# Kernel tuning notes

Hardware: AMD Instinct MI355X
Metric: run time of the kernel (lower is better)

Reference implementation:

```python
import jax, jax.numpy as jnp
import numpy as np

EMBED_DIM = 1024
N_HEADS = 16
HEAD_DIM = EMBED_DIM // N_HEADS


def setup_inputs() -> dict:
    key = jax.random.key(0)
    ks = jax.random.split(key, 9)
    s = 1.0 / np.sqrt(EMBED_DIM)
    x = jax.random.normal(ks[0], (4, 2048, EMBED_DIM), dtype=jnp.float32)
    Wq = jax.random.uniform(ks[1], (EMBED_DIM, EMBED_DIM), jnp.float32, -s, s)
    bq = jax.random.uniform(ks[2], (EMBED_DIM,), jnp.float32, -s, s)
    Wk = jax.random.uniform(ks[3], (EMBED_DIM, EMBED_DIM), jnp.float32, -s, s)
    bk = jax.random.uniform(ks[4], (EMBED_DIM,), jnp.float32, -s, s)
    Wv = jax.random.uniform(ks[5], (EMBED_DIM, EMBED_DIM), jnp.float32, -s, s)
    bv = jax.random.uniform(ks[6], (EMBED_DIM,), jnp.float32, -s, s)
    Wo = jax.random.uniform(ks[7], (EMBED_DIM, EMBED_DIM), jnp.float32, -s, s)
    bo = jax.random.uniform(ks[8], (EMBED_DIM,), jnp.float32, -s, s)
    return {"x": x, "Wq": Wq, "bq": bq, "Wk": Wk, "bk": bk,
            "Wv": Wv, "bv": bv, "Wo": Wo, "bo": bo}


def reference(x, Wq, bq, Wk, bk, Wv, bv, Wo, bo):
    B, S, _ = x.shape
    # projections (PyTorch Linear: x @ W.T + b; weights stored as [in,out] here)
    q = x @ Wq + bq
    k = x @ Wk + bk
    v = x @ Wv + bv
    # [B, H, S, D]
    q = q.reshape(B, S, N_HEADS, HEAD_DIM).transpose(0, 2, 1, 3)
    k = k.reshape(B, S, N_HEADS, HEAD_DIM).transpose(0, 2, 1, 3)
    v = v.reshape(B, S, N_HEADS, HEAD_DIM).transpose(0, 2, 1, 3)
    scores = jnp.einsum('bhsd,bhtd->bhst', q, k) / np.sqrt(HEAD_DIM).astype(np.float32)
    attn = jax.nn.softmax(scores, axis=-1)
    out = jnp.einsum('bhst,bhtd->bhsd', attn, v)
    out = out.transpose(0, 2, 1, 3).reshape(B, S, EMBED_DIM)
    return out @ Wo + bo  # dropout=0 (eval) -> identity
```

## Files before the change

### kernel.cpp

```cpp
#include <hip/hip_runtime.h>
#include <stdint.h>

#define EMBED 1024
#define NH 16
#define HD 64
#define SEQ 2048
#define BATCH 4
#define M_TOT (BATCH*SEQ)
#define QSCALE 0.18033688011112042f

typedef __attribute__((ext_vector_type(8))) short short8;
typedef __attribute__((ext_vector_type(4))) float floatx4;
typedef __attribute__((ext_vector_type(4))) unsigned int uintx4;

__device__ __forceinline__ unsigned short f2bf(float f) {
    union { float f; unsigned int u; } v; v.f = f;
    unsigned int r = v.u + 0x7fffu + ((v.u >> 16) & 1u);
    return (unsigned short)(r >> 16);
}

__device__ __forceinline__ void load_lds16(const unsigned short* g, unsigned short* l) {
    __builtin_amdgcn_global_load_lds(
        (const __attribute__((address_space(1))) unsigned int*)g,
        (__attribute__((address_space(3))) unsigned int*)l, 16, 0, 0);
}

__global__ void cvt_x(const float* __restrict__ x, unsigned short* __restrict__ xb) {
    int i = (blockIdx.x * 256 + threadIdx.x) * 4;
    float4 v = *(const float4*)(x + i);
    ushort4 o;
    o.x = f2bf(v.x); o.y = f2bf(v.y); o.z = f2bf(v.z); o.w = f2bf(v.w);
    *(ushort4*)(xb + i) = o;
}

__global__ void wtrans(const float* __restrict__ w0, const float* __restrict__ w1,
                       const float* __restrict__ w2, const float* __restrict__ w3,
                       unsigned short* __restrict__ t0, unsigned short* __restrict__ t1,
                       unsigned short* __restrict__ t2, unsigned short* __restrict__ t3) {
    __shared__ float tile[32][33];
    const float* W; unsigned short* T;
    switch (blockIdx.z) { case 0: W=w0; T=t0; break; case 1: W=w1; T=t1; break;
                          case 2: W=w2; T=t2; break; default: W=w3; T=t3; }
    int n0 = blockIdx.x * 32, k0 = blockIdx.y * 32;
    int tx = threadIdx.x, ty = threadIdx.y;
    #pragma unroll
    for (int i = 0; i < 4; i++)
        tile[ty + i*8][tx] = W[(k0 + ty + i*8) * EMBED + n0 + tx];
    __syncthreads();
    #pragma unroll
    for (int i = 0; i < 4; i++)
        T[(n0 + ty + i*8) * EMBED + k0 + tx] = f2bf(tile[tx][ty + i*8]);
}

#define ST_AH(buf_, kt_, h_) do { \
    const unsigned short* s_ = Asrc + (kt_)*64 + (h_)*64*EMBED; \
    unsigned short* d_ = ldst + (buf_)*32768 + (h_)*4096; \
    load_lds16(s_,              d_); \
    load_lds16(s_ + 128*EMBED,  d_ + 8192); \
  } while(0)
#define ST_BH(buf_, kt_, h_) do { \
    const unsigned short* s_ = Bsrc + (kt_)*64 + (h_)*32*EMBED; \
    unsigned short* d_ = bdst + (buf_)*32768 + (h_)*2048; \
    load_lds16(s_,              d_); \
    load_lds16(s_ + 128*EMBED,  d_ + 8192); \
  } while(0)

template<int MO, int NO>
__device__ __forceinline__ void mfma_quad(floatx4 (&acc)[8][4],
        const short8 (&a)[4][2], const short8 (&b)[2][2]) {
    #pragma unroll
    for (int k=0;k<2;k++)
      #pragma unroll
      for (int m=0;m<4;m++)
        #pragma unroll
        for (int n=0;n<2;n++)
          acc[MO+m][NO+n] = __builtin_amdgcn_mfma_f32_16x16x32_bf16(a[m][k], b[n][k], acc[MO+m][NO+n], 0,0,0);
}

template<bool B1, bool T2, int WAITN>
__device__ __forceinline__ void ktile(int t, int buf,
        const unsigned short* Abase, const unsigned short* Bbase,
        const unsigned short* Asrc, const unsigned short* Bsrc,
        unsigned short* ldst, unsigned short* bdst,
        int cs0, int cs1, floatx4 (&acc)[8][4]) {
    const unsigned short* Ab = Abase + buf*32768;
    const unsigned short* Bb = Bbase + buf*32768;
    short8 fA[4][2], fBlo[2][2], fBhi[2][2];
    #pragma unroll
    for (int i=0;i<4;i++) {
        fA[i][0] = *(const short8*)(Ab + i*1024 + cs0);
        fA[i][1] = *(const short8*)(Ab + i*1024 + cs1);
    }
    #pragma unroll
    for (int n=0;n<2;n++) {
        fBlo[n][0] = *(const short8*)(Bb + n*1024 + cs0);
        fBlo[n][1] = *(const short8*)(Bb + n*1024 + cs1);
    }
    if (B1) ST_BH(buf^1, t+1, 1);
    asm volatile("s_waitcnt lgkmcnt(8)");
    __builtin_amdgcn_s_barrier();
    asm volatile("s_waitcnt lgkmcnt(0)");
    __builtin_amdgcn_s_setprio(1);
    mfma_quad<0,0>(acc, fA, fBlo);
    __builtin_amdgcn_s_setprio(0);
    __builtin_amdgcn_s_barrier();
    #pragma unroll
    for (int n=0;n<2;n++) {
        fBhi[n][0] = *(const short8*)(Bb + (2+n)*1024 + cs0);
        fBhi[n][1] = *(const short8*)(Bb + (2+n)*1024 + cs1);
    }
    if (T2) ST_AH(buf, t+2, 0);
    __builtin_amdgcn_s_barrier();
    asm volatile("s_waitcnt lgkmcnt(0)");
    __builtin_amdgcn_s_setprio(1);
    mfma_quad<0,2>(acc, fA, fBhi);
    __builtin_amdgcn_s_setprio(0);
    __builtin_amdgcn_s_barrier();
    #pragma unroll
    for (int i=0;i<4;i++) {
        fA[i][0] = *(const short8*)(Ab + (4+i)*1024 + cs0);
        fA[i][1] = *(const short8*)(Ab + (4+i)*1024 + cs1);
    }
    if (T2) ST_BH(buf, t+2, 0);
    __builtin_amdgcn_s_barrier();
    asm volatile("s_waitcnt lgkmcnt(0)");
    __builtin_amdgcn_s_setprio(1);
    mfma_quad<4,2>(acc, fA, fBhi);
    __builtin_amdgcn_s_setprio(0);
    __builtin_amdgcn_s_barrier();
    if (T2) ST_AH(buf, t+2, 1);
    __builtin_amdgcn_s_setprio(1);
    mfma_quad<4,0>(acc, fA, fBlo);
    __builtin_amdgcn_s_setprio(0);
    if (WAITN == 6)      { asm volatile("s_waitcnt vmcnt(6)" ::: "memory"); }
    else if (WAITN == 0) { asm volatile("s_waitcnt vmcnt(0)" ::: "memory"); }
    __builtin_amdgcn_s_barrier();
}

__global__ __launch_bounds__(512, 2) void gemm8(
        const unsigned short* __restrict__ A, const unsigned short* __restrict__ BT,
        const float* __restrict__ b0, const float* __restrict__ b1, const float* __restrict__ b2,
        void* __restrict__ o0, void* __restrict__ o1, void* __restrict__ o2, int mode) {
    __shared__ unsigned short lds[2*32768];
    const int tid = threadIdx.x;
    const int lane = tid & 63, wave = tid >> 6;
    const int quad = lane >> 4, l16 = lane & 15;
    const int wm = wave >> 2, wn = wave & 3;
    const int id = blockIdx.x;
    const int xcd = id & 7, j = id >> 3;
    const int mblk = (xcd * 4 + (j & 3)) * 256;
    const int nblk = (j >> 2) * 256;

    const int srow = tid >> 3;
    const int scol = ((tid & 7) ^ (srow & 7)) * 8;
    const int brow = (srow & 31) + ((srow >> 5) << 6);
    const unsigned short* Asrc = A  + (size_t)(mblk + srow) * EMBED + scol;
    const unsigned short* Bsrc = BT + (size_t)(nblk + brow) * EMBED + scol;
    unsigned short* ldst = lds + wave * 512;
    unsigned short* bdst = lds + 16384 + (wave & 3)*512 + (wave >> 2)*4096;

    const int cs0 = ( quad      ^ (l16 & 7)) * 8;
    const int cs1 = ((quad ^ 4) ^ (l16 & 7)) * 8;
    const unsigned short* Abase = lds + (wm*128 + l16)*64;
    const unsigned short* Bbase = lds + 16384 + (wn*64 + l16)*64;

    floatx4 acc[8][4];
    #pragma unroll
    for (int m=0;m<8;m++)
      #pragma unroll
      for (int n=0;n<4;n++) acc[m][n] = (floatx4){0.f,0.f,0.f,0.f};

    ST_AH(0,0,0); ST_BH(0,0,0); ST_BH(0,0,1); ST_AH(0,0,1);
    asm volatile("s_waitcnt vmcnt(4)" ::: "memory");
    ST_AH(1,1,0); ST_BH(1,1,0); ST_AH(1,1,1);
    asm volatile("s_waitcnt vmcnt(6)" ::: "memory");
    __builtin_amdgcn_s_barrier();

    #pragma unroll 2
    for (int t = 0; t < 14; ++t)
        ktile<true, true, 6>(t, t & 1, Abase, Bbase, Asrc, Bsrc, ldst, bdst, cs0, cs1, acc);
    ktile<true,  false, 0>(14, 0, Abase, Bbase, Asrc, Bsrc, ldst, bdst, cs0, cs1, acc);
    ktile<false, false, -1>(15, 1, Abase, Bbase, Asrc, Bsrc, ldst, bdst, cs0, cs1, acc);

    if (mode == 1) {
        float* O = (float*)o0;
        #pragma unroll
        for (int mt=0;mt<8;mt++)
          #pragma unroll
          for (int nt=0;nt<4;nt++) {
            int col = nblk + wn*64 + nt*16 + l16;
            float bv = b0[col];
            #pragma unroll
            for (int r=0;r<4;r++) {
                int row = mblk + wm*128 + mt*16 + quad*4 + r;
                O[(size_t)row * EMBED + col] = acc[mt][nt][r] + bv;
            }
          }
    } else {
        int which = nblk >> 10;
        const float* bs = (which==0) ? b0 : (which==1) ? b1 : b2;
        unsigned short* O = (unsigned short*)((which==0) ? o0 : (which==1) ? o1 : o2);
        #pragma unroll
        for (int mt=0;mt<8;mt++)
          #pragma unroll
          for (int nt=0;nt<4;nt++) {
            int coll = (nblk & 1023) + wn*64 + nt*16 + l16;
            float bv = bs[coll];
            int h = coll >> 6, d = coll & 63;
            #pragma unroll
            for (int r=0;r<4;r++) {
                int row = mblk + wm*128 + mt*16 + quad*4 + r;
                int b = row >> 11, s = row & 2047;
                float v = acc[mt][nt][r] + bv;
                if (which == 0) {
                    v *= QSCALE;
                    O[((size_t)(b*NH + h)*SEQ + s)*HD + d] = f2bf(v);
                } else if (which == 1) {
                    O[((size_t)(b*NH + h)*SEQ + s)*HD + d] = f2bf(v);
                } else {
                    int sp = (s & ~31) | (((s >> 2) & 3) << 3) | (((s >> 4) & 1) << 2) | (s & 3);
                    O[((size_t)(b*NH + h)*HD + d)*SEQ + sp] = f2bf(v);
                }
            }
          }
    }
}

__global__ __launch_bounds__(512, 4) void attn(
    const unsigned short* __restrict__ Q, const unsigned short* __restrict__ K,
    const unsigned short* __restrict__ VTp, unsigned short* __restrict__ O) {
    __shared__ unsigned short kv[2][4096];
    unsigned short* kvf = &kv[0][0];
    int tid = threadIdx.x;
    int lane = tid & 63, wave = tid >> 6;
    int quad = lane >> 4, l16 = lane & 15;
    int id = blockIdx.x;
    int bh = (id & 7) * 8 + (id >> 6);
    int qblk = (id >> 3) & 7;
    int b = bh >> 4, h = bh & 15;
    int q0 = qblk * 256 + wave * 32;
    const unsigned short* Qb = Q + (size_t)bh * SEQ * HD;
    const unsigned short* Kb = K + (size_t)bh * SEQ * HD;
    const unsigned short* Vb = VTp + (size_t)bh * HD * SEQ;
    int li = (wave & 3) * 64 + lane;
    const unsigned short* src;
    int dstofs = (wave & 3) * 512 + ((wave >> 2) ? 2048 : 0);
    int src_step;
    if (wave < 4) {
        int t = li >> 3, slot = li & 7;
        int dblk = slot ^ (t & 7);
        src = Kb + (size_t)t * HD + dblk * 8;
        src_step = 32 * HD;
    } else {
        int d = li >> 2, slot = li & 3;
        int swz = (d & 3) ^ ((d >> 2) & 3);
        src = Vb + (size_t)d * SEQ + (slot ^ swz) * 8;
        src_step = 32;
    }
    short8 qf[2][2];
    #pragma unroll
    for (int mt=0;mt<2;mt++) {
        const unsigned short* qp = Qb + (size_t)(q0 + mt*16 + l16) * HD + quad*8;
        qf[mt][0] = *(const short8*)(qp);
        qf[mt][1] = *(const short8*)(qp + 32);
    }
    floatx4 o_acc[2][4], l_acc[2];
    #pragma unroll
    for (int mt=0;mt<2;mt++) {
        l_acc[mt] = (floatx4){0.f,0.f,0.f,0.f};
        #pragma unroll
        for (int dt=0;dt<4;dt++) o_acc[mt][dt] = (floatx4){0.f,0.f,0.f,0.f};
    }
    short8 ones;
    #pragma unroll
    for (int jj=0;jj<8;jj++) ones[jj] = (short)0x3F80;
    int koff[2][2], voff[4];
    #pragma unroll
    for (int nt=0;nt<2;nt++) {
        int t = nt*16 + l16;
        #pragma unroll
        for (int hh=0;hh<2;hh++)
            koff[nt][hh] = t*64 + ((hh*4 + quad) ^ (t & 7)) * 8;
    }
    #pragma unroll
    for (int dt=0;dt<4;dt++) {
        int d = dt*16 + l16;
        voff[dt] = 2048 + d*32 + ((quad ^ (d & 3) ^ ((d >> 2) & 3))) * 8;
    }

    load_lds16(src, kvf + dstofs);
    src += src_step;

    for (int it = 0; it < 64; ++it) {
        const unsigned short* kb = kvf + (it & 1) * 4096;
        if (it < 63) {
            load_lds16(src, kvf + ((it & 1) ^ 1) * 4096 + dstofs);
            src += src_step;
            asm volatile("s_waitcnt vmcnt(1)" ::: "memory");
        } else {
            asm volatile("s_waitcnt vmcnt(0)" ::: "memory");
        }
        __builtin_amdgcn_s_barrier();
        asm volatile("" ::: "memory");
        short8 kf[2][2], vf[4];
        #pragma unroll
        for (int nt=0;nt<2;nt++) {
            kf[nt][0] = *(const short8*)(kb + koff[nt][0]);
            kf[nt][1] = *(const short8*)(kb + koff[nt][1]);
        }
        #pragma unroll
        for (int dt=0;dt<4;dt++)
            vf[dt] = *(const short8*)(kb + voff[dt]);
        floatx4 sacc[2][2];
        __builtin_amdgcn_s_setprio(1);
        #pragma unroll
        for (int nt=0;nt<2;nt++)
          #pragma unroll
          for (int mt=0;mt<2;mt++) {
            floatx4 s = (floatx4){0.f,0.f,0.f,0.f};
            s = __builtin_amdgcn_mfma_f32_16x16x32_bf16(kf[nt][0], qf[mt][0], s, 0, 0, 0);
            s = __builtin_amdgcn_mfma_f32_16x16x32_bf16(kf[nt][1], qf[mt][1], s, 0, 0, 0);
            sacc[nt][mt] = s;
          }
        __builtin_amdgcn_s_setprio(0);
        short8 pf[2];
        #pragma unroll
        for (int mt=0;mt<2;mt++) {
            uintx4 pu;
            #pragma unroll
            for (int jp=0;jp<4;jp++) {
                int nt = jp >> 1, rp = (jp & 1) * 2;
                union { float f; unsigned int u; } e0, e1;
                e0.f = __builtin_amdgcn_exp2f(sacc[nt][mt][rp]);
                e1.f = __builtin_amdgcn_exp2f(sacc[nt][mt][rp+1]);
                pu[jp] = ((e1.u + 0x8000u) & 0xFFFF0000u) | ((e0.u + 0x8000u) >> 16);
            }
            pf[mt] = __builtin_bit_cast(short8, pu);
        }
        __builtin_amdgcn_s_setprio(1);
        #pragma unroll
        for (int mt=0;mt<2;mt++) {
            l_acc[mt] = __builtin_amdgcn_mfma_f32_16x16x32_bf16(ones, pf[mt], l_acc[mt], 0, 0, 0);
            #pragma unroll
            for (int dt=0;dt<4;dt++)
                o_acc[mt][dt] = __builtin_amdgcn_mfma_f32_16x16x32_bf16(vf[dt], pf[mt], o_acc[mt][dt], 0, 0, 0);
        }
        __builtin_amdgcn_s_setprio(0);
        asm volatile("" ::: "memory");
        __builtin_amdgcn_s_barrier();
    }
    #pragma unroll
    for (int mt=0;mt<2;mt++) {
        float inv = 1.f / l_acc[mt][0];
        int s = q0 + mt*16 + l16;
        #pragma unroll
        for (int dt=0;dt<4;dt++) {
            ushort4 w;
            w.x = f2bf(o_acc[mt][dt][0]*inv);
            w.y = f2bf(o_acc[mt][dt][1]*inv);
            w.z = f2bf(o_acc[mt][dt][2]*inv);
            w.w = f2bf(o_acc[mt][dt][3]*inv);
            *(ushort4*)(O + ((size_t)b*SEQ + s)*EMBED + h*HD + dt*16 + quad*4) = w;
        }
    }
}

extern "C" void kernel_launch(void* const* d_in, const int* in_sizes, int n_in,
                              void* d_out, int out_size, void* d_ws, size_t ws_size,
                              hipStream_t stream) {
    const float* x  = (const float*)d_in[0];
    const float* Wq = (const float*)d_in[1]; const float* bq = (const float*)d_in[2];
    const float* Wk = (const float*)d_in[3]; const float* bk = (const float*)d_in[4];
    const float* Wv = (const float*)d_in[5]; const float* bv = (const float*)d_in[6];
    const float* Wo = (const float*)d_in[7]; const float* bo = (const float*)d_in[8];
    char* ws = (char*)d_ws;
    unsigned short* xb  = (unsigned short*)(ws);
    unsigned short* WqT = (unsigned short*)(ws + (16ull<<20));
    unsigned short* WkT = (unsigned short*)(ws + (18ull<<20));
    unsigned short* WvT = (unsigned short*)(ws + (20ull<<20));
    unsigned short* WoT = (unsigned short*)(ws + (22ull<<20));
    unsigned short* Qb  = (unsigned short*)(ws + (24ull<<20));
    unsigned short* Kb  = (unsigned short*)(ws + (40ull<<20));
    unsigned short* VTb = (unsigned short*)(ws + (56ull<<20));
    unsigned short* Ob  = xb;

    cvt_x<<<(M_TOT*EMBED)/1024, 256, 0, stream>>>(x, xb);
    wtrans<<<dim3(32,32,4), dim3(32,8), 0, stream>>>(Wq,Wk,Wv,Wo, WqT,WkT,WvT,WoT);
    gemm8<<<dim3(384), 512, 0, stream>>>(xb, WqT, bq, bk, bv, Qb, Kb, VTb, 0);
    attn<<<dim3(512), 512, 0, stream>>>(Qb, Kb, VTb, Ob);
    gemm8<<<dim3(128), 512, 0, stream>>>(Ob, WoT, bo, bo, bo, (float*)d_out, nullptr, nullptr, 1);
}
```

Measured before the change: 289.1 us.

## Rewrite projection GEMM with 32-wide K tiles, 4-stage LDS ring, LDS-staged V transpose

The GEMM main loop now uses K-steps of 32 over a 4-buffer LDS ring with 3 tiles in flight. Each step takes a single vmcnt wait and barrier, replacing the old 64-wide double-buffered loop with its many interleaved barriers and setprio phases. The V-projection epilogue now writes its transposed, permuted output through an LDS staging tile so global stores are coalesced 16-byte vectors instead of scattered 2-byte writes. The mode is also made a template parameter. The cost is more loop iterations and a changed swizzle, and the new LDS bank pattern or load issue could hurt MFMA overlap.

```diff
diff --git a/kernel.cpp b/kernel.cpp
--- a/kernel.cpp
+++ b/kernel.cpp
@@ -52,96 +52,47 @@
         T[(n0 + ty + i*8) * EMBED + k0 + tx] = f2bf(tile[tx][ty + i*8]);
 }
 
-#define ST_AH(buf_, kt_, h_) do { \
-    const unsigned short* s_ = Asrc + (kt_)*64 + (h_)*64*EMBED; \
-    unsigned short* d_ = ldst + (buf_)*32768 + (h_)*4096; \
-    load_lds16(s_,              d_); \
-    load_lds16(s_ + 128*EMBED,  d_ + 8192); \
+#define ST32(kt_) do { \
+    const int b_ = (kt_) & 3; \
+    const unsigned short* sa_ = Asrc + (kt_)*32; \
+    const unsigned short* sb_ = Bsrc + (kt_)*32; \
+    unsigned short* da_ = ldstA + b_*16384; \
+    unsigned short* db_ = ldstB + b_*16384; \
+    load_lds16(sa_,             da_); \
+    load_lds16(sa_ + 128*EMBED, da_ + 4096); \
+    load_lds16(sb_,             db_); \
+    load_lds16(sb_ + 128*EMBED, db_ + 4096); \
   } while(0)
-#define ST_BH(buf_, kt_, h_) do { \
-    const unsigned short* s_ = Bsrc + (kt_)*64 + (h_)*32*EMBED; \
-    unsigned short* d_ = bdst + (buf_)*32768 + (h_)*2048; \
-    load_lds16(s_,              d_); \
-    load_lds16(s_ + 128*EMBED,  d_ + 8192); \
-  } while(0)
-
-template<int MO, int NO>
-__device__ __forceinline__ void mfma_quad(floatx4 (&acc)[8][4],
-        const short8 (&a)[4][2], const short8 (&b)[2][2]) {
-    #pragma unroll
-    for (int k=0;k<2;k++)
-      #pragma unroll
-      for (int m=0;m<4;m++)
-        #pragma unroll
-        for (int n=0;n<2;n++)
-          acc[MO+m][NO+n] = __builtin_amdgcn_mfma_f32_16x16x32_bf16(a[m][k], b[n][k], acc[MO+m][NO+n], 0,0,0);
-}
-
-template<bool B1, bool T2, int WAITN>
-__device__ __forceinline__ void ktile(int t, int buf,
+
+template<int WAITN, bool STG>
+__device__ __forceinline__ void kt32(int t,
         const unsigned short* Abase, const unsigned short* Bbase,
         const unsigned short* Asrc, const unsigned short* Bsrc,
-        unsigned short* ldst, unsigned short* bdst,
-        int cs0, int cs1, floatx4 (&acc)[8][4]) {
-    const unsigned short* Ab = Abase + buf*32768;
-    const unsigned short* Bb = Bbase + buf*32768;
-    short8 fA[4][2], fBlo[2][2], fBhi[2][2];
-    #pragma unroll
-    for (int i=0;i<4;i++) {
-        fA[i][0] = *(const short8*)(Ab + i*1024 + cs0);
-        fA[i][1] = *(const short8*)(Ab + i*1024 + cs1);
-    }
-    #pragma unroll
-    for (int n=0;n<2;n++) {
-        fBlo[n][0] = *(const short8*)(Bb + n*1024 + cs0);
-        fBlo[n][1] = *(const short8*)(Bb + n*1024 + cs1);
-    }
-    if (B1) ST_BH(buf^1, t+1, 1);
-    asm volatile("s_waitcnt lgkmcnt(8)");
-    __builtin_amdgcn_s_barrier();
-    asm volatile("s_waitcnt lgkmcnt(0)");
-    __builtin_amdgcn_s_setprio(1);
-    mfma_quad<0,0>(acc, fA, fBlo);
-    __builtin_amdgcn_s_setprio(0);
-    __builtin_amdgcn_s_barrier();
-    #pragma unroll
-    for (int n=0;n<2;n++) {
-        fBhi[n][0] = *(const short8*)(Bb + (2+n)*1024 + cs0);
-        fBhi[n][1] = *(const short8*)(Bb + (2+n)*1024 + cs1);
-    }
-    if (T2) ST_AH(buf, t+2, 0);
-    __builtin_amdgcn_s_barrier();
-    asm volatile("s_waitcnt lgkmcnt(0)");
-    __builtin_amdgcn_s_setprio(1);
-    mfma_quad<0,2>(acc, fA, fBhi);
-    __builtin_amdgcn_s_setprio(0);
-    __builtin_amdgcn_s_barrier();
-    #pragma unroll
-    for (int i=0;i<4;i++) {
-        fA[i][0] = *(const short8*)(Ab + (4+i)*1024 + cs0);
-        fA[i][1] = *(const short8*)(Ab + (4+i)*1024 + cs1);
-    }
-    if (T2) ST_BH(buf, t+2, 0);
-    __builtin_amdgcn_s_barrier();
-    asm volatile("s_waitcnt lgkmcnt(0)");
-    __builtin_amdgcn_s_setprio(1);
-    mfma_quad<4,2>(acc, fA, fBhi);
-    __builtin_amdgcn_s_setprio(0);
-    __builtin_amdgcn_s_barrier();
-    if (T2) ST_AH(buf, t+2, 1);
-    __builtin_amdgcn_s_setprio(1);
-    mfma_quad<4,0>(acc, fA, fBlo);
-    __builtin_amdgcn_s_setprio(0);
-    if (WAITN == 6)      { asm volatile("s_waitcnt vmcnt(6)" ::: "memory"); }
-    else if (WAITN == 0) { asm volatile("s_waitcnt vmcnt(0)" ::: "memory"); }
-    __builtin_amdgcn_s_barrier();
-}
-
-__global__ __launch_bounds__(512, 2) void gemm8(
+        unsigned short* ldstA, unsigned short* ldstB, floatx4 (&acc)[8][4]) {
+    const int bo = (t & 3) * 16384;
+    short8 fA[8], fB[4];
+    #pragma unroll
+    for (int m=0;m<8;m++) fA[m] = *(const short8*)(Abase + bo + m*512);
+    #pragma unroll
+    for (int n=0;n<4;n++) fB[n] = *(const short8*)(Bbase + bo + n*512);
+    if (STG) ST32(t+3);
+    #pragma unroll
+    for (int m=0;m<8;m++)
+      #pragma unroll
+      for (int n=0;n<4;n++)
+        acc[m][n] = __builtin_amdgcn_mfma_f32_16x16x32_bf16(fA[m], fB[n], acc[m][n], 0,0,0);
+    if (WAITN >= 0) {
+        asm volatile("s_waitcnt vmcnt(%0)" :: "i"(WAITN >= 0 ? WAITN : 0) : "memory");
+        asm volatile("s_barrier" ::: "memory");
+    }
+}
+
+template<int MODE>
+__global__ __launch_bounds__(512, 2) void gemm32(
         const unsigned short* __restrict__ A, const unsigned short* __restrict__ BT,
         const float* __restrict__ b0, const float* __restrict__ b1, const float* __restrict__ b2,
-        void* __restrict__ o0, void* __restrict__ o1, void* __restrict__ o2, int mode) {
-    __shared__ unsigned short lds[2*32768];
+        void* __restrict__ o0, void* __restrict__ o1, void* __restrict__ o2) {
+    __shared__ unsigned short lds[4*16384];
     const int tid = threadIdx.x;
     const int lane = tid & 63, wave = tid >> 6;
     const int quad = lane >> 4, l16 = lane & 15;
@@ -151,18 +102,16 @@
     const int mblk = (xcd * 4 + (j & 3)) * 256;
     const int nblk = (j >> 2) * 256;
 
-    const int srow = tid >> 3;
-    const int scol = ((tid & 7) ^ (srow & 7)) * 8;
-    const int brow = (srow & 31) + ((srow >> 5) << 6);
+    const int srow = tid >> 2;
+    const int scol = ((tid & 3) ^ (srow & 3)) * 8;
     const unsigned short* Asrc = A  + (size_t)(mblk + srow) * EMBED + scol;
-    const unsigned short* Bsrc = BT + (size_t)(nblk + brow) * EMBED + scol;
-    unsigned short* ldst = lds + wave * 512;
-    unsigned short* bdst = lds + 16384 + (wave & 3)*512 + (wave >> 2)*4096;
-
-    const int cs0 = ( quad      ^ (l16 & 7)) * 8;
-    const int cs1 = ((quad ^ 4) ^ (l16 & 7)) * 8;
-    const unsigned short* Abase = lds + (wm*128 + l16)*64;
-    const unsigned short* Bbase = lds + 16384 + (wn*64 + l16)*64;
+    const unsigned short* Bsrc = BT + (size_t)(nblk + srow) * EMBED + scol;
+    unsigned short* ldstA = lds + wave * 512;
+    unsigned short* ldstB = lds + 8192 + wave * 512;
+
+    const int cs = (quad ^ (l16 & 3)) * 8;
+    const unsigned short* Abase = lds + (wm*128 + l16)*32 + cs;
+    const unsigned short* Bbase = lds + 8192 + (wn*64 + l16)*32 + cs;
 
     floatx4 acc[8][4];
     #pragma unroll
@@ -170,19 +119,19 @@
       #pragma unroll
       for (int n=0;n<4;n++) acc[m][n] = (floatx4){0.f,0.f,0.f,0.f};
 
-    ST_AH(0,0,0); ST_BH(0,0,0); ST_BH(0,0,1); ST_AH(0,0,1);
-    asm volatile("s_waitcnt vmcnt(4)" ::: "memory");
-    ST_AH(1,1,0); ST_BH(1,1,0); ST_AH(1,1,1);
-    asm volatile("s_waitcnt vmcnt(6)" ::: "memory");
-    __builtin_amdgcn_s_barrier();
-
-    #pragma unroll 2
-    for (int t = 0; t < 14; ++t)
-        ktile<true, true, 6>(t, t & 1, Abase, Bbase, Asrc, Bsrc, ldst, bdst, cs0, cs1, acc);
-    ktile<true,  false, 0>(14, 0, Abase, Bbase, Asrc, Bsrc, ldst, bdst, cs0, cs1, acc);
-    ktile<false, false, -1>(15, 1, Abase, Bbase, Asrc, Bsrc, ldst, bdst, cs0, cs1, acc);
-
-    if (mode == 1) {
+    ST32(0); ST32(1); ST32(2);
+    asm volatile("s_waitcnt vmcnt(8)" ::: "memory");
+    asm volatile("s_barrier" ::: "memory");
+
+    #pragma unroll 4
+    for (int t = 0; t < 28; ++t)
+        kt32<8,true>(t, Abase, Bbase, Asrc, Bsrc, ldstA, ldstB, acc);
+    kt32<8,true >(28, Abase, Bbase, Asrc, Bsrc, ldstA, ldstB, acc);
+    kt32<4,false>(29, Abase, Bbase, Asrc, Bsrc, ldstA, ldstB, acc);
+    kt32<0,false>(30, Abase, Bbase, Asrc, Bsrc, ldstA, ldstB, acc);
+    kt32<-1,false>(31, Abase, Bbase, Asrc, Bsrc, ldstA, ldstB, acc);
+
+    if (MODE == 1) {
         float* O = (float*)o0;
         #pragma unroll
         for (int mt=0;mt<8;mt++)
@@ -199,30 +148,55 @@
     } else {
         int which = nblk >> 10;
         const float* bs = (which==0) ? b0 : (which==1) ? b1 : b2;
-        unsigned short* O = (unsigned short*)((which==0) ? o0 : (which==1) ? o1 : o2);
-        #pragma unroll
-        for (int mt=0;mt<8;mt++)
-          #pragma unroll
-          for (int nt=0;nt<4;nt++) {
-            int coll = (nblk & 1023) + wn*64 + nt*16 + l16;
-            float bv = bs[coll];
-            int h = coll >> 6, d = coll & 63;
-            #pragma unroll
-            for (int r=0;r<4;r++) {
-                int row = mblk + wm*128 + mt*16 + quad*4 + r;
-                int b = row >> 11, s = row & 2047;
-                float v = acc[mt][nt][r] + bv;
-                if (which == 0) {
-                    v *= QSCALE;
-                    O[((size_t)(b*NH + h)*SEQ + s)*HD + d] = f2bf(v);
-                } else if (which == 1) {
-                    O[((size_t)(b*NH + h)*SEQ + s)*HD + d] = f2bf(v);
-                } else {
-                    int sp = (s & ~31) | (((s >> 2) & 3) << 3) | (((s >> 4) & 1) << 2) | (s & 3);
-                    O[((size_t)(b*NH + h)*HD + d)*SEQ + sp] = f2bf(v);
+        if (which < 2) {
+            unsigned short* O = (unsigned short*)((which==0) ? o0 : o1);
+            float sc = (which==0) ? QSCALE : 1.f;
+            #pragma unroll
+            for (int mt=0;mt<8;mt++)
+              #pragma unroll
+              for (int nt=0;nt<4;nt++) {
+                int coll = (nblk & 1023) + wn*64 + nt*16 + l16;
+                float bv = bs[coll];
+                int h = coll >> 6, d = coll & 63;
+                #pragma unroll
+                for (int r=0;r<4;r++) {
+                    int row = mblk + wm*128 + mt*16 + quad*4 + r;
+                    int b = row >> 11, s = row & 2047;
+                    O[((size_t)(b*NH + h)*SEQ + s)*HD + d] = f2bf((acc[mt][nt][r] + bv) * sc);
+                }
+              }
+        } else {
+            unsigned short* T = lds;
+            __syncthreads();
+            #pragma unroll
+            for (int nt=0;nt<4;nt++) {
+                int cloc = wn*64 + nt*16 + l16;
+                float bv = bs[(nblk & 1023) + cloc];
+                int sw = (cloc & 3) << 3;
+                #pragma unroll
+                for (int mt=0;mt<8;mt++) {
+                    int row0 = wm*128 + mt*16 + quad*4;
+                    int sp0 = (row0 & ~31) | (((row0 >> 2) & 3) << 3) | (((row0 >> 4) & 1) << 2);
+                    ushort4 w;
+                    w.x = f2bf(acc[mt][nt][0] + bv);
+                    w.y = f2bf(acc[mt][nt][1] + bv);
+                    w.z = f2bf(acc[mt][nt][2] + bv);
+                    w.w = f2bf(acc[mt][nt][3] + bv);
+                    *(ushort4*)(T + cloc*256 + (sp0 ^ sw)) = w;
                 }
             }
-          }
+            __syncthreads();
+            unsigned short* OV = (unsigned short*)o2;
+            int s0 = (lane & 31) * 8, dloc = lane >> 5;
+            size_t rowbase = ((size_t)((mblk >> 11)*1024 + (nblk & 1023))) * SEQ + (mblk & 2047);
+            #pragma unroll
+            for (int i=0;i<16;i++) {
+                int c = wave*32 + i*2 + dloc;
+                int sw2 = (c & 3) << 3;
+                short8 v = *(const short8*)(T + c*256 + (s0 ^ sw2));
+                *(short8*)(OV + rowbase + (size_t)c * SEQ + s0) = v;
+            }
+        }
     }
 }
 
@@ -386,7 +360,7 @@
 
     cvt_x<<<(M_TOT*EMBED)/1024, 256, 0, stream>>>(x, xb);
     wtrans<<<dim3(32,32,4), dim3(32,8), 0, stream>>>(Wq,Wk,Wv,Wo, WqT,WkT,WvT,WoT);
-    gemm8<<<dim3(384), 512, 0, stream>>>(xb, WqT, bq, bk, bv, Qb, Kb, VTb, 0);
+    gemm32<0><<<dim3(384), 512, 0, stream>>>(xb, WqT, bq, bk, bv, Qb, Kb, VTb);
     attn<<<dim3(512), 512, 0, stream>>>(Qb, Kb, VTb, Ob);
-    gemm8<<<dim3(128), 512, 0, stream>>>(Ob, WoT, bo, bo, bo, (float*)d_out, nullptr, nullptr, 1);
-}
+    gemm32<1><<<dim3(128), 512, 0, stream>>>(Ob, WoT, bo, bo, bo, (float*)d_out, nullptr, nullptr);
+}
```

New measurement: 267.7 us. 1.08x faster.
